# Performance work log

Measured on AMD Instinct MI355X. Metric: run time of the kernel, lower is better.

## Reference

```python
import jax, jax.numpy as jnp
import numpy as np

NUM_PATCHES_SIDE = 32
LOCAL_RADIUS = 3.0


def _build_non_local_mask():
    # coords of each patch on the grid, matching torch.meshgrid(indexing='ij')
    h = np.arange(NUM_PATCHES_SIDE)
    hh, ww = np.meshgrid(h, h, indexing='ij')
    coors = np.stack([hh, ww], axis=0).astype(np.float32)  # (2, H, W)
    coors = coors.reshape(2, -1).T                          # (n, 2)
    dist = np.linalg.norm(coors[:, None, :] - coors[None, :, :], axis=-1)
    return jnp.asarray(dist > LOCAL_RADIUS)                 # (n, n) bool


def setup_inputs() -> dict:
    key = jax.random.key(0)
    b, n, l, d = 8, NUM_PATCHES_SIDE * NUM_PATCHES_SIDE, 6, 512
    levels = jax.random.normal(key, (b, n, l, d), dtype=jnp.float32)
    non_local_mask = _build_non_local_mask()
    return {"levels": levels, "non_local_mask": non_local_mask}


def reference(levels, non_local_mask):
    b, n, l, d = levels.shape
    # F.normalize(levels, dim=-1): x / max(||x||, eps)
    norm = jnp.linalg.norm(levels, axis=-1, keepdims=True)
    k = levels / jnp.maximum(norm, 1e-12)
    # scores per level: (b, l, n, n)
    sim = jnp.einsum('bild,bjld->blij', levels, k) * (d ** -0.5)
    max_neg = -jnp.finfo(sim.dtype).max
    sim = jnp.where(non_local_mask[None, None, :, :], max_neg, sim)
    attn = jax.nn.softmax(sim, axis=-1)
    out = jnp.einsum('blij,bjld->bild', attn, levels)
    return out
```

## Files before the change

kernel.cpp:

```cpp
#include <hip/hip_runtime.h>
#include <math.h>

#define NPS 32
#define NN  (NPS*NPS)
#define LL  6
#define DD  512
#define NBR 28

#define INV_SQRT_D 0.044194173824159216f
#define LOG2E      1.4426950408889634f
#define KLOG       (INV_SQRT_D * LOG2E)

__device__ __forceinline__ float wave_sum_bcast(float x) {
    int t;
    t = __builtin_amdgcn_update_dpp(0, __float_as_int(x), 0xB1, 0xF, 0xF, true);
    x += __int_as_float(t);
    t = __builtin_amdgcn_update_dpp(0, __float_as_int(x), 0x4E, 0xF, 0xF, true);
    x += __int_as_float(t);
    t = __builtin_amdgcn_update_dpp(0, __float_as_int(x), 0x141, 0xF, 0xF, true);
    x += __int_as_float(t);
    t = __builtin_amdgcn_update_dpp(0, __float_as_int(x), 0x140, 0xF, 0xF, true);
    x += __int_as_float(t);
    x += __int_as_float(__builtin_amdgcn_ds_swizzle(__float_as_int(x), 0x401F));
    x += __shfl_xor(x, 32, 64);
    return x;
}

__global__ __launch_bounds__(256) void ca_norm_kernel(const float* __restrict__ levels,
                                                      float* __restrict__ cws, int rows) {
    int w = (int)(blockIdx.x * 4 + (threadIdx.x >> 6));
    if (w >= rows) return;
    int lane = threadIdx.x & 63;
    const float4* x4 = (const float4*)(levels + (size_t)w * DD);
    float4 a0 = x4[lane * 2];
    float4 a1 = x4[lane * 2 + 1];
    float s2 = a0.x*a0.x + a0.y*a0.y + a0.z*a0.z + a0.w*a0.w
             + a1.x*a1.x + a1.y*a1.y + a1.z*a1.z + a1.w*a1.w;
    s2 = wave_sum_bcast(s2);
    if (lane == 0) cws[w] = KLOG * __frsqrt_rn(s2);
}

template<bool USE_C>
__global__ __launch_bounds__(256) void ca_fused2(const float* __restrict__ levels,
                                                 const float* __restrict__ cws,
                                                 float* __restrict__ out, int rows) {
    constexpr int dh[NBR] = {-3,
                             -2,-2,-2,-2,-2,
                             -1,-1,-1,-1,-1,
                              0, 0, 0, 0, 0, 0,
                              1, 1, 1, 1, 1,
                              2, 2, 2, 2, 2,
                              3};
    constexpr int dw[NBR] = { 0,
                             -2,-1, 0, 1, 2,
                             -2,-1, 0, 1, 2,
                             -3,-2,-1, 1, 2, 3,
                             -2,-1, 0, 1, 2,
                             -2,-1, 0, 1, 2,
                              0};

    unsigned bk    = blockIdx.x;
    unsigned chunk = gridDim.x >> 3;
    unsigned vb    = (bk & 7) * chunk + (bk >> 3);
    int w = __builtin_amdgcn_readfirstlane((int)(vb * 4 + (threadIdx.x >> 6)));
    if (w >= rows) return;
    int lane = threadIdx.x & 63;

    int i  = (w / LL) % NN;
    int ph = i >> 5;
    int pw = i & 31;

    const float4* xi4 = (const float4*)(levels + (size_t)w * DD);
    int l2 = lane * 2;
    float4 a0 = xi4[l2];
    float4 a1 = xi4[l2 + 1];

    float m2;
    if constexpr (USE_C) {
        m2 = (KLOG * KLOG) / cws[w];
    } else {
        float s2i = a0.x*a0.x + a0.y*a0.y + a0.z*a0.z + a0.w*a0.w
                  + a1.x*a1.x + a1.y*a1.y + a1.z*a1.z + a1.w*a1.w;
        s2i = wave_sum_bcast(s2i);
        m2  = __fsqrt_rn(s2i) * KLOG;
    }

    float lsum = 1.0f;
    float acc0 = a0.x, acc1 = a0.y, acc2 = a0.z, acc3 = a0.w;
    float acc4 = a1.x, acc5 = a1.y, acc6 = a1.z, acc7 = a1.w;

    #pragma unroll
    for (int t = 0; t < NBR; ++t) {
        int hh = ph + dh[t];
        int ww = pw + dw[t];
        if ((unsigned)hh < (unsigned)NPS && (unsigned)ww < (unsigned)NPS) {
            int jrow = w + (dh[t] * NPS + dw[t]) * LL;
            const float4* xj4 = (const float4*)(levels + (size_t)jrow * DD);
            float4 b0 = xj4[l2];
            float4 b1 = xj4[l2 + 1];
            float d = a0.x * b0.x;
            d = fmaf(a0.y, b0.y, d); d = fmaf(a0.z, b0.z, d); d = fmaf(a0.w, b0.w, d);
            d = fmaf(a1.x, b1.x, d); d = fmaf(a1.y, b1.y, d); d = fmaf(a1.z, b1.z, d);
            d = fmaf(a1.w, b1.w, d);
            d = wave_sum_bcast(d);
            float cj;
            if constexpr (USE_C) {
                cj = cws[jrow];
            } else {
                float s2 = b0.x*b0.x + b0.y*b0.y + b0.z*b0.z + b0.w*b0.w
                         + b1.x*b1.x + b1.y*b1.y + b1.z*b1.z + b1.w*b1.w;
                s2 = wave_sum_bcast(s2);
                cj = KLOG * __frsqrt_rn(s2);
            }
            float p = __builtin_amdgcn_exp2f(fmaf(d, cj, -m2));
            lsum += p;
            acc0 = fmaf(p, b0.x, acc0); acc1 = fmaf(p, b0.y, acc1);
            acc2 = fmaf(p, b0.z, acc2); acc3 = fmaf(p, b0.w, acc3);
            acc4 = fmaf(p, b1.x, acc4); acc5 = fmaf(p, b1.y, acc5);
            acc6 = fmaf(p, b1.z, acc6); acc7 = fmaf(p, b1.w, acc7);
        }
    }

    float inv = 1.0f / lsum;
    float4 o0 = make_float4(acc0 * inv, acc1 * inv, acc2 * inv, acc3 * inv);
    float4 o1 = make_float4(acc4 * inv, acc5 * inv, acc6 * inv, acc7 * inv);
    float4* o4 = (float4*)(out + (size_t)w * DD);
    o4[l2]     = o0;
    o4[l2 + 1] = o1;
}

extern "C" void kernel_launch(void* const* d_in, const int* in_sizes, int n_in,
                              void* d_out, int out_size, void* d_ws, size_t ws_size,
                              hipStream_t stream) {
    const float* levels = (const float*)d_in[0];
    float* out = (float*)d_out;

    int rows   = in_sizes[0] / DD;
    int blocks = (rows + 3) / 4;

    if (d_ws && ws_size >= (size_t)rows * sizeof(float)) {
        float* cws = (float*)d_ws;
        ca_norm_kernel<<<blocks, 256, 0, stream>>>(levels, cws, rows);
        ca_fused2<true><<<blocks, 256, 0, stream>>>(levels, cws, out, rows);
    } else {
        ca_fused2<false><<<blocks, 256, 0, stream>>>(levels, nullptr, out, rows);
    }
}
```

Baseline: 254.1 us.

## Split each wave into two half-waves processing neighbor pairs, reorder block-to-row mapping

```diff
diff --git a/kernel.cpp b/kernel.cpp
--- a/kernel.cpp
+++ b/kernel.cpp
@@ -5,13 +5,14 @@
 #define NN  (NPS*NPS)
 #define LL  6
 #define DD  512
-#define NBR 28
+#define ROWSPB (NN*LL)
+#define BIAS 576
 
 #define INV_SQRT_D 0.044194173824159216f
 #define LOG2E      1.4426950408889634f
 #define KLOG       (INV_SQRT_D * LOG2E)
 
-__device__ __forceinline__ float wave_sum_bcast(float x) {
+__device__ __forceinline__ float half_sum32(float x) {
     int t;
     t = __builtin_amdgcn_update_dpp(0, __float_as_int(x), 0xB1, 0xF, 0xF, true);
     x += __int_as_float(t);
@@ -22,96 +23,189 @@
     t = __builtin_amdgcn_update_dpp(0, __float_as_int(x), 0x140, 0xF, 0xF, true);
     x += __int_as_float(t);
     x += __int_as_float(__builtin_amdgcn_ds_swizzle(__float_as_int(x), 0x401F));
+    return x;
+}
+
+__device__ __forceinline__ float wave_sum_bcast(float x) {
+    x = half_sum32(x);
     x += __shfl_xor(x, 32, 64);
     return x;
 }
 
-__global__ __launch_bounds__(256) void ca_norm_kernel(const float* __restrict__ levels,
-                                                      float* __restrict__ cws, int rows) {
-    int w = (int)(blockIdx.x * 4 + (threadIdx.x >> 6));
+__global__ __launch_bounds__(256) void ca_norm2(const float* __restrict__ levels,
+                                                float* __restrict__ cws,
+                                                float* __restrict__ mws, int rows) {
+    int tid  = threadIdx.x;
+    int lane = tid & 63;
+    int sl   = lane & 31;
+    int grp  = lane >> 5;
+    int w = ((int)blockIdx.x * 4 + (tid >> 6)) * 2 + grp;
     if (w >= rows) return;
-    int lane = threadIdx.x & 63;
-    const float4* x4 = (const float4*)(levels + (size_t)w * DD);
-    float4 a0 = x4[lane * 2];
-    float4 a1 = x4[lane * 2 + 1];
+    const float4* x4 = (const float4*)(levels + (unsigned)(w * DD));
+    float4 a0 = x4[sl*4+0], a1 = x4[sl*4+1], a2 = x4[sl*4+2], a3 = x4[sl*4+3];
     float s2 = a0.x*a0.x + a0.y*a0.y + a0.z*a0.z + a0.w*a0.w
-             + a1.x*a1.x + a1.y*a1.y + a1.z*a1.z + a1.w*a1.w;
-    s2 = wave_sum_bcast(s2);
-    if (lane == 0) cws[w] = KLOG * __frsqrt_rn(s2);
-}
-
-template<bool USE_C>
-__global__ __launch_bounds__(256) void ca_fused2(const float* __restrict__ levels,
+             + a1.x*a1.x + a1.y*a1.y + a1.z*a1.z + a1.w*a1.w
+             + a2.x*a2.x + a2.y*a2.y + a2.z*a2.z + a2.w*a2.w
+             + a3.x*a3.x + a3.y*a3.y + a3.z*a3.z + a3.w*a3.w;
+    s2 = half_sum32(s2);
+    if (sl == 0) {
+        float r = __frsqrt_rn(s2);
+        cws[w] = KLOG * r;
+        mws[w] = KLOG * s2 * r;
+    }
+}
+
+__global__ __launch_bounds__(256) void ca_fused3(const float* __restrict__ levels,
                                                  const float* __restrict__ cws,
+                                                 const float* __restrict__ mws,
                                                  float* __restrict__ out, int rows) {
-    constexpr int dh[NBR] = {-3,
-                             -2,-2,-2,-2,-2,
-                             -1,-1,-1,-1,-1,
-                              0, 0, 0, 0, 0, 0,
-                              1, 1, 1, 1, 1,
-                              2, 2, 2, 2, 2,
-                              3};
-    constexpr int dw[NBR] = { 0,
-                             -2,-1, 0, 1, 2,
-                             -2,-1, 0, 1, 2,
-                             -3,-2,-1, 1, 2, 3,
-                             -2,-1, 0, 1, 2,
-                             -2,-1, 0, 1, 2,
-                              0};
-
+    constexpr int dhA[14] = {-3,-2,-2,-1,-1,-1, 0, 0, 0, 1, 1, 2, 2, 2};
+    constexpr int dwA[14] = { 0,-1, 1,-2, 0, 2,-2, 1, 3,-1, 1,-2, 0, 2};
+    constexpr int dhB[14] = {-2,-2,-2,-1,-1, 0, 0, 0, 1, 1, 1, 2, 2, 3};
+    constexpr int dwB[14] = {-2, 0, 2,-1, 1,-3,-1, 2,-2, 0, 2,-1, 1, 0};
+
+    unsigned bk    = blockIdx.x;
+    unsigned chunk = gridDim.x >> 3;
+    unsigned vb    = (bk & 7) * chunk + (bk >> 3);
+
+    int tid  = threadIdx.x;
+    int lane = tid & 63;
+    int sl   = lane & 31;
+    bool hi  = lane >= 32;
+
+    int b  = (int)(vb / 1536u);
+    int r1 = (int)(vb - (unsigned)b * 1536u);
+    int pg = r1 / 6;
+    int l  = r1 - pg * 6;
+    int p  = __builtin_amdgcn_readfirstlane(pg * 4 + (tid >> 6));
+    int w  = __builtin_amdgcn_readfirstlane(b * ROWSPB + p * LL + l);
+    if (w >= rows) return;
+    int ph = p >> 5;
+    int pw = p & 31;
+
+    const float4* xi4 = (const float4*)(levels + (size_t)w * DD);
+    float4 a0 = xi4[sl*4+0], a1 = xi4[sl*4+1], a2 = xi4[sl*4+2], a3 = xi4[sl*4+3];
+
+    float m2 = mws[w];
+
+    float  lsum = 0.0f;
+    float4 c0 = make_float4(0.f,0.f,0.f,0.f);
+    float4 c1 = make_float4(0.f,0.f,0.f,0.f);
+    float4 c2 = make_float4(0.f,0.f,0.f,0.f);
+    float4 c3 = make_float4(0.f,0.f,0.f,0.f);
+
+    const char* lvb   = (const char*)levels + ((long long)w - BIAS) * (DD * 4);
+    const char* cwb   = (const char*)cws    + ((long long)w - BIAS) * 4;
+    int laneoff = sl * 64;
+
+    #pragma unroll
+    for (int t = 0; t < 14; ++t) {
+        int hA = ph + dhA[t], wA = pw + dwA[t];
+        int hB = ph + dhB[t], wB = pw + dwB[t];
+        bool vA = ((unsigned)hA < NPS) && ((unsigned)wA < NPS);
+        bool vB = ((unsigned)hB < NPS) && ((unsigned)wB < NPS);
+        if (vA | vB) {
+            int roffA = vA ? (dhA[t] * NPS + dwA[t]) * LL : 0;
+            int roffB = vB ? (dhB[t] * NPS + dwB[t]) * LL : 0;
+            int offA  = (roffA + BIAS) * (DD * 4);
+            int offB  = (roffB + BIAS) * (DD * 4);
+            int off   = hi ? offB : offA;
+            const float4* bp = (const float4*)(lvb + off + laneoff);
+            float4 b0 = bp[0], b1 = bp[1], b2 = bp[2], b3 = bp[3];
+            float cj = *(const float*)(cwb + (off >> 9));
+
+            float d;
+            d = a0.x * b0.x;
+            d = fmaf(a0.y, b0.y, d); d = fmaf(a0.z, b0.z, d); d = fmaf(a0.w, b0.w, d);
+            d = fmaf(a1.x, b1.x, d); d = fmaf(a1.y, b1.y, d); d = fmaf(a1.z, b1.z, d);
+            d = fmaf(a1.w, b1.w, d);
+            d = fmaf(a2.x, b2.x, d); d = fmaf(a2.y, b2.y, d); d = fmaf(a2.z, b2.z, d);
+            d = fmaf(a2.w, b2.w, d);
+            d = fmaf(a3.x, b3.x, d); d = fmaf(a3.y, b3.y, d); d = fmaf(a3.z, b3.z, d);
+            d = fmaf(a3.w, b3.w, d);
+            d = half_sum32(d);
+
+            float pr = __builtin_amdgcn_exp2f(fmaf(d, cj, -m2));
+            bool myv = hi ? vB : vA;
+            pr = myv ? pr : 0.0f;
+            lsum += pr;
+            c0.x = fmaf(pr, b0.x, c0.x); c0.y = fmaf(pr, b0.y, c0.y);
+            c0.z = fmaf(pr, b0.z, c0.z); c0.w = fmaf(pr, b0.w, c0.w);
+            c1.x = fmaf(pr, b1.x, c1.x); c1.y = fmaf(pr, b1.y, c1.y);
+            c1.z = fmaf(pr, b1.z, c1.z); c1.w = fmaf(pr, b1.w, c1.w);
+            c2.x = fmaf(pr, b2.x, c2.x); c2.y = fmaf(pr, b2.y, c2.y);
+            c2.z = fmaf(pr, b2.z, c2.z); c2.w = fmaf(pr, b2.w, c2.w);
+            c3.x = fmaf(pr, b3.x, c3.x); c3.y = fmaf(pr, b3.y, c3.y);
+            c3.z = fmaf(pr, b3.z, c3.z); c3.w = fmaf(pr, b3.w, c3.w);
+        }
+    }
+
+    lsum += __shfl_xor(lsum, 32, 64);
+    c0.x += __shfl_xor(c0.x, 32, 64); c0.y += __shfl_xor(c0.y, 32, 64);
+    c0.z += __shfl_xor(c0.z, 32, 64); c0.w += __shfl_xor(c0.w, 32, 64);
+    c1.x += __shfl_xor(c1.x, 32, 64); c1.y += __shfl_xor(c1.y, 32, 64);
+    c1.z += __shfl_xor(c1.z, 32, 64); c1.w += __shfl_xor(c1.w, 32, 64);
+    c2.x += __shfl_xor(c2.x, 32, 64); c2.y += __shfl_xor(c2.y, 32, 64);
+    c2.z += __shfl_xor(c2.z, 32, 64); c2.w += __shfl_xor(c2.w, 32, 64);
+    c3.x += __shfl_xor(c3.x, 32, 64); c3.y += __shfl_xor(c3.y, 32, 64);
+    c3.z += __shfl_xor(c3.z, 32, 64); c3.w += __shfl_xor(c3.w, 32, 64);
+
+    lsum += 1.0f;
+    c0.x += a0.x; c0.y += a0.y; c0.z += a0.z; c0.w += a0.w;
+    c1.x += a1.x; c1.y += a1.y; c1.z += a1.z; c1.w += a1.w;
+    c2.x += a2.x; c2.y += a2.y; c2.z += a2.z; c2.w += a2.w;
+    c3.x += a3.x; c3.y += a3.y; c3.z += a3.z; c3.w += a3.w;
+
+    if (!hi) {
+        float inv = 1.0f / lsum;
+        float4* o4 = (float4*)(out + (size_t)w * DD);
+        o4[sl*4+0] = make_float4(c0.x*inv, c0.y*inv, c0.z*inv, c0.w*inv);
+        o4[sl*4+1] = make_float4(c1.x*inv, c1.y*inv, c1.z*inv, c1.w*inv);
+        o4[sl*4+2] = make_float4(c2.x*inv, c2.y*inv, c2.z*inv, c2.w*inv);
+        o4[sl*4+3] = make_float4(c3.x*inv, c3.y*inv, c3.z*inv, c3.w*inv);
+    }
+}
+
+__global__ __launch_bounds__(256) void ca_fallback(const float* __restrict__ levels,
+                                                   float* __restrict__ out, int rows) {
+    constexpr int dh[28] = {-3,-2,-2,-2,-2,-2,-1,-1,-1,-1,-1, 0, 0, 0, 0, 0, 0,
+                             1, 1, 1, 1, 1, 2, 2, 2, 2, 2, 3};
+    constexpr int dw[28] = { 0,-2,-1, 0, 1, 2,-2,-1, 0, 1, 2,-3,-2,-1, 1, 2, 3,
+                            -2,-1, 0, 1, 2,-2,-1, 0, 1, 2, 0};
     unsigned bk    = blockIdx.x;
     unsigned chunk = gridDim.x >> 3;
     unsigned vb    = (bk & 7) * chunk + (bk >> 3);
     int w = __builtin_amdgcn_readfirstlane((int)(vb * 4 + (threadIdx.x >> 6)));
     if (w >= rows) return;
     int lane = threadIdx.x & 63;
-
     int i  = (w / LL) % NN;
-    int ph = i >> 5;
-    int pw = i & 31;
-
+    int ph = i >> 5, pw = i & 31;
     const float4* xi4 = (const float4*)(levels + (size_t)w * DD);
     int l2 = lane * 2;
-    float4 a0 = xi4[l2];
-    float4 a1 = xi4[l2 + 1];
-
-    float m2;
-    if constexpr (USE_C) {
-        m2 = (KLOG * KLOG) / cws[w];
-    } else {
-        float s2i = a0.x*a0.x + a0.y*a0.y + a0.z*a0.z + a0.w*a0.w
-                  + a1.x*a1.x + a1.y*a1.y + a1.z*a1.z + a1.w*a1.w;
-        s2i = wave_sum_bcast(s2i);
-        m2  = __fsqrt_rn(s2i) * KLOG;
-    }
-
+    float4 a0 = xi4[l2], a1 = xi4[l2 + 1];
+    float s2i = a0.x*a0.x + a0.y*a0.y + a0.z*a0.z + a0.w*a0.w
+              + a1.x*a1.x + a1.y*a1.y + a1.z*a1.z + a1.w*a1.w;
+    s2i = wave_sum_bcast(s2i);
+    float m2 = __fsqrt_rn(s2i) * KLOG;
     float lsum = 1.0f;
-    float acc0 = a0.x, acc1 = a0.y, acc2 = a0.z, acc3 = a0.w;
-    float acc4 = a1.x, acc5 = a1.y, acc6 = a1.z, acc7 = a1.w;
-
+    float acc0=a0.x, acc1=a0.y, acc2=a0.z, acc3=a0.w;
+    float acc4=a1.x, acc5=a1.y, acc6=a1.z, acc7=a1.w;
     #pragma unroll
-    for (int t = 0; t < NBR; ++t) {
-        int hh = ph + dh[t];
-        int ww = pw + dw[t];
+    for (int t = 0; t < 28; ++t) {
+        int hh = ph + dh[t], ww = pw + dw[t];
         if ((unsigned)hh < (unsigned)NPS && (unsigned)ww < (unsigned)NPS) {
             int jrow = w + (dh[t] * NPS + dw[t]) * LL;
             const float4* xj4 = (const float4*)(levels + (size_t)jrow * DD);
-            float4 b0 = xj4[l2];
-            float4 b1 = xj4[l2 + 1];
+            float4 b0 = xj4[l2], b1 = xj4[l2 + 1];
             float d = a0.x * b0.x;
             d = fmaf(a0.y, b0.y, d); d = fmaf(a0.z, b0.z, d); d = fmaf(a0.w, b0.w, d);
             d = fmaf(a1.x, b1.x, d); d = fmaf(a1.y, b1.y, d); d = fmaf(a1.z, b1.z, d);
             d = fmaf(a1.w, b1.w, d);
             d = wave_sum_bcast(d);
-            float cj;
-            if constexpr (USE_C) {
-                cj = cws[jrow];
-            } else {
-                float s2 = b0.x*b0.x + b0.y*b0.y + b0.z*b0.z + b0.w*b0.w
-                         + b1.x*b1.x + b1.y*b1.y + b1.z*b1.z + b1.w*b1.w;
-                s2 = wave_sum_bcast(s2);
-                cj = KLOG * __frsqrt_rn(s2);
-            }
+            float q2 = b0.x*b0.x + b0.y*b0.y + b0.z*b0.z + b0.w*b0.w
+                     + b1.x*b1.x + b1.y*b1.y + b1.z*b1.z + b1.w*b1.w;
+            q2 = wave_sum_bcast(q2);
+            float cj = KLOG * __frsqrt_rn(q2);
             float p = __builtin_amdgcn_exp2f(fmaf(d, cj, -m2));
             lsum += p;
             acc0 = fmaf(p, b0.x, acc0); acc1 = fmaf(p, b0.y, acc1);
@@ -120,13 +214,10 @@
             acc6 = fmaf(p, b1.z, acc6); acc7 = fmaf(p, b1.w, acc7);
         }
     }
-
     float inv = 1.0f / lsum;
-    float4 o0 = make_float4(acc0 * inv, acc1 * inv, acc2 * inv, acc3 * inv);
-    float4 o1 = make_float4(acc4 * inv, acc5 * inv, acc6 * inv, acc7 * inv);
     float4* o4 = (float4*)(out + (size_t)w * DD);
-    o4[l2]     = o0;
-    o4[l2 + 1] = o1;
+    o4[l2]     = make_float4(acc0*inv, acc1*inv, acc2*inv, acc3*inv);
+    o4[l2 + 1] = make_float4(acc4*inv, acc5*inv, acc6*inv, acc7*inv);
 }
 
 extern "C" void kernel_launch(void* const* d_in, const int* in_sizes, int n_in,
@@ -135,14 +226,17 @@
     const float* levels = (const float*)d_in[0];
     float* out = (float*)d_out;
 
-    int rows   = in_sizes[0] / DD;
-    int blocks = (rows + 3) / 4;
-
-    if (d_ws && ws_size >= (size_t)rows * sizeof(float)) {
+    int rows = in_sizes[0] / DD;
+
+    if (d_ws && ws_size >= (size_t)rows * 2 * sizeof(float)) {
         float* cws = (float*)d_ws;
-        ca_norm_kernel<<<blocks, 256, 0, stream>>>(levels, cws, rows);
-        ca_fused2<true><<<blocks, 256, 0, stream>>>(levels, cws, out, rows);
+        float* mws = cws + rows;
+        int blocks1 = (rows + 7) / 8;
+        ca_norm2<<<blocks1, 256, 0, stream>>>(levels, cws, mws, rows);
+        int blocks2 = rows / 4;
+        ca_fused3<<<blocks2, 256, 0, stream>>>(levels, cws, mws, out, rows);
     } else {
-        ca_fused2<false><<<blocks, 256, 0, stream>>>(levels, nullptr, out, rows);
-    }
-}
+        int blocks = (rows + 3) / 4;
+        ca_fallback<<<blocks, 256, 0, stream>>>(levels, out, rows);
+    }
+}
```

Result: slower. 330.5 us (+30.1%).
